# Kernel optimization log

Hardware: AMD Instinct MI355X
Metric: run time of the kernel (lower is better)

Reference implementation:

```python
import jax, jax.numpy as jnp
import numpy as np

D_MODEL = 2048
NUM_HEADS = 16
HEAD_DIM = 128
BATCH = 4
SEQ = 2048


def setup_inputs() -> dict:
    key = jax.random.key(0)
    ks = jax.random.split(key, 5)
    s = 0.02
    return {
        "x": jax.random.normal(ks[0], (BATCH, SEQ, D_MODEL), dtype=jnp.float32),
        "Wq": jax.random.normal(ks[1], (NUM_HEADS * HEAD_DIM, D_MODEL), dtype=jnp.float32) * s,
        "Wk": jax.random.normal(ks[2], (NUM_HEADS * HEAD_DIM, D_MODEL), dtype=jnp.float32) * s,
        "Wv": jax.random.normal(ks[3], (NUM_HEADS * HEAD_DIM, D_MODEL), dtype=jnp.float32) * s,
        "Wo": jax.random.normal(ks[4], (D_MODEL, NUM_HEADS * HEAD_DIM), dtype=jnp.float32) * s,
    }


def _split_heads(t):
    b, s, _ = t.shape
    return t.reshape(b, s, NUM_HEADS, HEAD_DIM).transpose(0, 2, 1, 3)  # [b,h,s,d]


def reference(x, Wq, Wk, Wv, Wo):
    # prefill: QKV proj + causal SDPA + output proj. torch Linear: x @ W.T
    q = _split_heads(x @ Wq.T)
    k = _split_heads(x @ Wk.T)
    v = _split_heads(x @ Wv.T)
    scale = 1.0 / jnp.sqrt(jnp.asarray(HEAD_DIM, dtype=x.dtype))
    scores = jnp.einsum("bhqd,bhkd->bhqk", q, k) * scale
    causal = jnp.tril(jnp.ones((SEQ, SEQ), dtype=bool))
    scores = jnp.where(causal, scores, jnp.finfo(scores.dtype).min)
    attn = jax.nn.softmax(scores, axis=-1)
    y = jnp.einsum("bhqk,bhkd->bhqd", attn, v)
    y = y.transpose(0, 2, 1, 3).reshape(x.shape[0], SEQ, NUM_HEADS * HEAD_DIM)
    y = y @ Wo.T
    return (y, k, v)
```

## Files before the change

### kernel.cpp

```cpp
#include <hip/hip_runtime.h>
#include <stdint.h>

#define DM 2048
#define NH 16
#define HD 128
#define BB 4
#define SS 2048
#define BS (BB*SS)
#define NQKV (3*DM)
#define SCQ 0.12751744565f

typedef __bf16 bf16_t;
typedef __attribute__((ext_vector_type(8))) __bf16 bf16x8;
typedef __attribute__((ext_vector_type(4))) float f32x4;
typedef __attribute__((ext_vector_type(16))) float f32x16;
typedef __attribute__((ext_vector_type(4))) float float4v;
typedef __attribute__((ext_vector_type(4))) unsigned int uint4v;
typedef __attribute__((ext_vector_type(4))) unsigned short ushort4v;
typedef __attribute__((ext_vector_type(8))) unsigned short ushort8;

__device__ __forceinline__ unsigned short f2bf(float f) {
  unsigned u = __float_as_uint(f);
  u += 0x7fffu + ((u >> 16) & 1u);
  return (unsigned short)(u >> 16);
}

__device__ __forceinline__ void gl16(const void* g, void* l) {
  __builtin_amdgcn_global_load_lds(
      (const __attribute__((address_space(1))) unsigned int*)(unsigned long long)g,
      (__attribute__((address_space(3))) unsigned int*)(unsigned int)(unsigned long long)l,
      16, 0, 0);
}

#define DSR(dst, addr, IMM)                                                   \
  asm volatile("ds_read_b128 %0, %1 offset:" IMM : "=v"(dst) : "v"(addr))

__global__ void conv_f32_bf16(const float* __restrict__ in,
                              unsigned short* __restrict__ out, int n4) {
  int i = blockIdx.x * blockDim.x + threadIdx.x;
  int stride = gridDim.x * blockDim.x;
  for (; i < n4; i += stride) {
    float4v v = ((const float4v*)in)[i];
    ushort4v o;
    o.x = f2bf(v.x); o.y = f2bf(v.y); o.z = f2bf(v.z); o.w = f2bf(v.w);
    ((ushort4v*)out)[i] = o;
  }
}

template<int MODE>
__global__ __launch_bounds__(512)
void gemmr4(const bf16_t* __restrict__ A, const bf16_t* __restrict__ Bm,
            const int K, const int N, const int nbx,
            float* __restrict__ Cf, bf16_t* __restrict__ qbf,
            bf16_t* __restrict__ kbt, float* __restrict__ kf,
            float* __restrict__ vf, bf16_t* __restrict__ vtb) {
  __shared__ bf16_t As[4][256 * 32];
  __shared__ bf16_t Bs[4][256 * 32];
  const int t = threadIdx.x, w = t >> 6, lane = t & 63;
  const int fr = lane & 15, fq = lane >> 4;
  const int cpx = gridDim.x >> 3;
  const int orig = blockIdx.x;
  const int wg = (orig & 7) * cpx + (orig >> 3);
  const int bm = wg % nbx, bn = wg / nbx;
  const int row0 = bm * 256, col0 = bn * 256;
  const int wm = (w >> 2) * 128, wn = (w & 3) * 64;

  const bf16_t* Asrc[2];
  const bf16_t* Bsrc[2];
  int dst[2];
#pragma unroll
  for (int j = 0; j < 2; ++j) {
    int u = j * 512 + t, r = u >> 2, c = u & 3;
    Asrc[j] = A + (size_t)(row0 + r) * K + ((c ^ (r & 3)) * 8);
    Bsrc[j] = Bm + (size_t)(col0 + r) * K + ((c ^ (r & 3)) * 8);
    dst[j] = u * 16;
  }
  const int NT = K >> 5;
  f32x4 acc[8][4] = {};

  const unsigned As0 = (unsigned)(unsigned long long)(const void*)&As[0][0];
  const unsigned Bs0 = (unsigned)(unsigned long long)(const void*)&Bs[0][0];
  const unsigned xorc = (unsigned)((fq ^ (fr & 3)) << 4);
  const unsigned aoff = (unsigned)((wm + fr) * 64) + xorc;
  const unsigned boff = (unsigned)((wn + fr) * 64) + xorc;

#define STAGE(TT)                                                  \
  {                                                                \
    const int sl_ = (TT) & 3;                                      \
    const size_t ko_ = (size_t)(TT) * 32;                          \
    gl16(Asrc[0] + ko_, (char*)(&As[sl_][0]) + dst[0]);            \
    gl16(Asrc[1] + ko_, (char*)(&As[sl_][0]) + dst[1]);            \
    gl16(Bsrc[0] + ko_, (char*)(&Bs[sl_][0]) + dst[0]);            \
    gl16(Bsrc[1] + ko_, (char*)(&Bs[sl_][0]) + dst[1]);            \
  }

#define MFQUAD(FI, AV)                                                        \
  acc[FI][0] = __builtin_amdgcn_mfma_f32_16x16x32_bf16(                       \
      __builtin_bit_cast(bf16x8, AV), __builtin_bit_cast(bf16x8, bv0), acc[FI][0], 0, 0, 0); \
  acc[FI][1] = __builtin_amdgcn_mfma_f32_16x16x32_bf16(                       \
      __builtin_bit_cast(bf16x8, AV), __builtin_bit_cast(bf16x8, bv1), acc[FI][1], 0, 0, 0); \
  acc[FI][2] = __builtin_amdgcn_mfma_f32_16x16x32_bf16(                       \
      __builtin_bit_cast(bf16x8, AV), __builtin_bit_cast(bf16x8, bv2), acc[FI][2], 0, 0, 0); \
  acc[FI][3] = __builtin_amdgcn_mfma_f32_16x16x32_bf16(                       \
      __builtin_bit_cast(bf16x8, AV), __builtin_bit_cast(bf16x8, bv3), acc[FI][3], 0, 0, 0);

  STAGE(0); STAGE(1); STAGE(2);

  for (int T = 0; T < NT; ++T) {
    if (T + 2 < NT) {
      asm volatile("s_waitcnt vmcnt(8)" ::: "memory");
    } else if (T + 1 < NT) {
      asm volatile("s_waitcnt vmcnt(4)" ::: "memory");
    } else {
      asm volatile("s_waitcnt vmcnt(0)" ::: "memory");
    }
    asm volatile("s_barrier" ::: "memory");
    if (T + 3 < NT) STAGE(T + 3);

    const unsigned ab = As0 + (unsigned)(T & 3) * 16384 + aoff;
    const unsigned bb = Bs0 + (unsigned)(T & 3) * 16384 + boff;
    uint4v bv0, bv1, bv2, bv3, a0, a1, a2, a3, a4, a5, a6, a7;
    DSR(bv0, bb, "0");    DSR(bv1, bb, "1024");
    DSR(bv2, bb, "2048"); DSR(bv3, bb, "3072");
    DSR(a0, ab, "0");     DSR(a1, ab, "1024");
    DSR(a2, ab, "2048");  DSR(a3, ab, "3072");
    DSR(a4, ab, "4096");  DSR(a5, ab, "5120");
    DSR(a6, ab, "6144");  DSR(a7, ab, "7168");

    asm volatile("s_waitcnt lgkmcnt(4)" ::: "memory");
    __builtin_amdgcn_sched_barrier(0);
    __builtin_amdgcn_s_setprio(1);
    MFQUAD(0, a0) MFQUAD(1, a1) MFQUAD(2, a2) MFQUAD(3, a3)
    __builtin_amdgcn_s_setprio(0);

    asm volatile("s_waitcnt lgkmcnt(0)" ::: "memory");
    __builtin_amdgcn_sched_barrier(0);
    __builtin_amdgcn_s_setprio(1);
    MFQUAD(4, a4) MFQUAD(5, a5) MFQUAD(6, a6) MFQUAD(7, a7)
    __builtin_amdgcn_s_setprio(0);
  }
#undef STAGE
#undef MFQUAD

#pragma unroll
  for (int f = 0; f < 8; ++f) {
#pragma unroll
    for (int jn = 0; jn < 4; ++jn) {
#pragma unroll
      for (int r = 0; r < 4; ++r) {
        int m = row0 + wm + f * 16 + fq * 4 + r;
        int n = col0 + wn + jn * 16 + fr;
        float v = acc[f][jn][r];
        if (MODE == 0) {
          Cf[(size_t)m * N + n] = v;
        } else {
          int b = m >> 11, s = m & 2047;
          if (n < DM) {
            int h = n >> 7, d = n & 127;
            qbf[(((size_t)(b * NH + h)) * SS + s) * HD + d] = (bf16_t)(v * SCQ);
          } else if (n < 2 * DM) {
            int nn = n - DM, h = nn >> 7, d = nn & 127;
            size_t o = (((size_t)(b * NH + h)) * SS + s) * HD + d;
            kbt[o] = (bf16_t)v;
            kf[o] = v;
          } else {
            int nn = n - 2 * DM, h = nn >> 7, d = nn & 127;
            size_t o = (((size_t)(b * NH + h)) * SS + s) * HD + d;
            vf[o] = v;
            vtb[((size_t)(b * NH + h)) * (HD * SS) + (size_t)d * SS + s] = (bf16_t)v;
          }
        }
      }
    }
  }
}

__global__ __launch_bounds__(256, 2)
void attn_fwd4(const bf16_t* __restrict__ qbf, const bf16_t* __restrict__ kbf,
               const bf16_t* __restrict__ vt, bf16_t* __restrict__ aout) {
  __shared__ bf16_t Ks[2][64 * 128];
  __shared__ bf16_t Vs[2][64 * 128];
  const int t = threadIdx.x, w = t >> 6, lane = t & 63;
  const int l31 = lane & 31, hi = lane >> 5;
  const int orig = blockIdx.x;
  const int wg = (orig & 7) * 128 + (orig >> 3);
  const int bh = wg >> 4;
  const int qt = 15 - (wg & 15);
  const int q0 = qt * 128;
  const int nt = 2 * qt + 2;
  const size_t bh_off = (size_t)bh * SS * HD;
  const char* kbase = (const char*)(kbf + bh_off);
  const char* vbase = (const char*)(vt + bh_off);

  const char* ksrc[4];
  const char* vsrc[4];
#pragma unroll
  for (int i = 0; i < 4; ++i) {
    int r = (w * 4 + i) * 4 + (lane >> 4);
    int c = (lane & 15) ^ (r & 15);
    ksrc[i] = kbase + r * 256 + c * 16;
    int d = 2 * r + (c >> 3);
    vsrc[i] = vbase + (size_t)d * (SS * 2) + (c & 7) * 16;
  }

  bf16x8 qfr[8];
  {
    const char* qrow = (const char*)(qbf + bh_off + (size_t)(q0 + w * 32 + l31) * HD);
#pragma unroll
    for (int ds = 0; ds < 8; ++ds)
      qfr[ds] = *(const bf16x8*)(qrow + ds * 32 + hi * 16);
  }

#pragma unroll
  for (int i = 0; i < 4; ++i) {
    gl16(ksrc[i], (char*)(&Ks[0][0]) + (w * 4 + i) * 1024);
    gl16(vsrc[i], (char*)(&Vs[0][0]) + (w * 4 + i) * 1024);
    ksrc[i] += 16384;
    vsrc[i] += 128;
  }

  float mrow = -3.0e38f, lrow = 0.f;
  f32x16 accO[4] = {};

  auto make_pa = [&](const f32x16& sv, bf16x8& paA, bf16x8& paB) {
    unsigned W[8];
#pragma unroll
    for (int m = 0; m < 8; ++m) {
      float lo = sv[2 * m], hh = sv[2 * m + 1];
      asm("v_cvt_pk_bf16_f32 %0, %1, %2" : "=v"(W[m]) : "v"(lo), "v"(hh));
    }
#pragma unroll
    for (int g = 0; g < 2; ++g) {
      unsigned A = W[4 * g], B = W[4 * g + 1], C = W[4 * g + 2], D = W[4 * g + 3];
      unsigned xA = (unsigned)__shfl_xor((int)A, 32, 64);
      unsigned xB = (unsigned)__shfl_xor((int)B, 32, 64);
      unsigned xC = (unsigned)__shfl_xor((int)C, 32, 64);
      unsigned xD = (unsigned)__shfl_xor((int)D, 32, 64);
      uint4v u;
      u.x = hi ? xC : A;
      u.y = hi ? xD : B;
      u.z = hi ? C : xA;
      u.w = hi ? D : xB;
      if (g == 0) paA = __builtin_bit_cast(bf16x8, u);
      else        paB = __builtin_bit_cast(bf16x8, u);
    }
  };

  for (int kt = 0; kt < nt; ++kt) {
    const int cur = kt & 1;
    __syncthreads();

    if (kt + 1 < nt) {
#pragma unroll
      for (int i = 0; i < 4; ++i) {
        gl16(ksrc[i], (char*)(&Ks[cur ^ 1][0]) + (w * 4 + i) * 1024);
        gl16(vsrc[i], (char*)(&Vs[cur ^ 1][0]) + (w * 4 + i) * 1024);
        ksrc[i] += 16384;
        vsrc[i] += 128;
      }
    }

    const char* kl = (const char*)&Ks[cur][0];
    f32x16 s0 = {}, s1 = {};
    const int rck = l31 & 15;
    __builtin_amdgcn_s_setprio(1);
#pragma unroll
    for (int ds = 0; ds < 8; ++ds) {
      int ch = ((2 * ds + hi) ^ rck) << 4;
      bf16x8 kf0 = *(const bf16x8*)(kl + l31 * 256 + ch);
      s0 = __builtin_amdgcn_mfma_f32_32x32x16_bf16(kf0, qfr[ds], s0, 0, 0, 0);
      bf16x8 kf1 = *(const bf16x8*)(kl + (32 + l31) * 256 + ch);
      s1 = __builtin_amdgcn_mfma_f32_32x32x16_bf16(kf1, qfr[ds], s1, 0, 0, 0);
    }
    __builtin_amdgcn_s_setprio(0);

    const int kv0 = kt * 64;
    if (kt >= 2 * qt) {
      const int qg = q0 + w * 32 + l31;
#pragma unroll
      for (int r = 0; r < 16; ++r) {
        int klo = kv0 + (r & 3) + 8 * (r >> 2) + 4 * hi;
        if (klo > qg) s0[r] = -3.0e38f;
        if (klo + 32 > qg) s1[r] = -3.0e38f;
      }
    }
    float rm = s0[0];
#pragma unroll
    for (int r = 1; r < 16; ++r) rm = fmaxf(rm, s0[r]);
#pragma unroll
    for (int r = 0; r < 16; ++r) rm = fmaxf(rm, s1[r]);
    rm = fmaxf(rm, __shfl_xor(rm, 32, 64));
    if (__ballot(rm > mrow + 8.0f)) {
      float mnew = fmaxf(mrow, rm);
      float fct = __builtin_amdgcn_exp2f(mrow - mnew);
      mrow = mnew;
      lrow *= fct;
#pragma unroll
      for (int r = 0; r < 16; ++r) {
        float f = __shfl(fct, (r & 3) + 8 * (r >> 2) + 4 * hi, 64);
        accO[0][r] *= f; accO[1][r] *= f; accO[2][r] *= f; accO[3][r] *= f;
      }
    }
    float ss = 0.f;
#pragma unroll
    for (int r = 0; r < 16; ++r) { float p = __builtin_amdgcn_exp2f(s0[r] - mrow); s0[r] = p; ss += p; }
#pragma unroll
    for (int r = 0; r < 16; ++r) { float p = __builtin_amdgcn_exp2f(s1[r] - mrow); s1[r] = p; ss += p; }
    ss += __shfl_xor(ss, 32, 64);
    lrow += ss;

    bf16x8 pa00, pa01, pa10, pa11;
    make_pa(s0, pa00, pa01);
    make_pa(s1, pa10, pa11);

    const char* vl = (const char*)&Vs[cur][0];
    __builtin_amdgcn_s_setprio(1);
#pragma unroll
    for (int dt = 0; dt < 4; ++dt) {
      int R = dt * 16 + (l31 >> 1);
      int cb = (l31 & 1) << 3;
      int rx = R & 15;
      bf16x8 v00 = *(const bf16x8*)(vl + R * 256 + (((cb + 0 + hi) ^ rx) << 4));
      accO[dt] = __builtin_amdgcn_mfma_f32_32x32x16_bf16(pa00, v00, accO[dt], 0, 0, 0);
      bf16x8 v01 = *(const bf16x8*)(vl + R * 256 + (((cb + 2 + hi) ^ rx) << 4));
      accO[dt] = __builtin_amdgcn_mfma_f32_32x32x16_bf16(pa01, v01, accO[dt], 0, 0, 0);
      bf16x8 v10 = *(const bf16x8*)(vl + R * 256 + (((cb + 4 + hi) ^ rx) << 4));
      accO[dt] = __builtin_amdgcn_mfma_f32_32x32x16_bf16(pa10, v10, accO[dt], 0, 0, 0);
      bf16x8 v11 = *(const bf16x8*)(vl + R * 256 + (((cb + 6 + hi) ^ rx) << 4));
      accO[dt] = __builtin_amdgcn_mfma_f32_32x32x16_bf16(pa11, v11, accO[dt], 0, 0, 0);
    }
    __builtin_amdgcn_s_setprio(0);
  }

  const int b = bh >> 4, h = bh & 15;
#pragma unroll
  for (int r = 0; r < 16; ++r) {
    int qr = (r & 3) + 8 * (r >> 2) + 4 * hi;
    float inv = __builtin_amdgcn_rcpf(__shfl(lrow, qr, 64));
    int srow = q0 + w * 32 + qr;
    bf16_t* orow = aout + ((size_t)(b * SS + srow)) * DM + h * HD + l31;
    orow[0]  = (bf16_t)(accO[0][r] * inv);
    orow[32] = (bf16_t)(accO[1][r] * inv);
    orow[64] = (bf16_t)(accO[2][r] * inv);
    orow[96] = (bf16_t)(accO[3][r] * inv);
  }
}

extern "C" void kernel_launch(void* const* d_in, const int* in_sizes, int n_in,
                              void* d_out, int out_size, void* d_ws, size_t ws_size,
                              hipStream_t stream) {
  (void)in_sizes; (void)n_in; (void)out_size; (void)ws_size;
  const float* x  = (const float*)d_in[0];
  const float* Wq = (const float*)d_in[1];
  const float* Wk = (const float*)d_in[2];
  const float* Wv = (const float*)d_in[3];
  const float* Wo = (const float*)d_in[4];

  float* y  = (float*)d_out;
  float* kf = y + (size_t)BS * DM;
  float* vf = kf + (size_t)BS * DM;

  char* ws = (char*)d_ws;
  bf16_t* xbf  = (bf16_t*)ws;
  bf16_t* abf  = xbf;
  bf16_t* qbf  = (bf16_t*)(ws + (size_t)32 * 1024 * 1024);
  bf16_t* wobf = qbf;
  bf16_t* wqkv = (bf16_t*)(ws + (size_t)64 * 1024 * 1024);
  bf16_t* kbt  = (bf16_t*)y;
  bf16_t* vtb  = (bf16_t*)((char*)y + (size_t)32 * 1024 * 1024);

  conv_f32_bf16<<<2048, 256, 0, stream>>>(x, (unsigned short*)xbf, BS * DM / 4);
  conv_f32_bf16<<<512, 256, 0, stream>>>(Wq, (unsigned short*)wqkv, DM * DM / 4);
  conv_f32_bf16<<<512, 256, 0, stream>>>(Wk, (unsigned short*)(wqkv + (size_t)DM * DM), DM * DM / 4);
  conv_f32_bf16<<<512, 256, 0, stream>>>(Wv, (unsigned short*)(wqkv + 2 * (size_t)DM * DM), DM * DM / 4);

  gemmr4<1><<<768, 512, 0, stream>>>(
      xbf, wqkv, DM, NQKV, 32, nullptr, qbf, kbt, kf, vf, vtb);

  attn_fwd4<<<1024, 256, 0, stream>>>(qbf, kbt, vtb, abf);

  conv_f32_bf16<<<512, 256, 0, stream>>>(Wo, (unsigned short*)wobf, DM * DM / 4);

  gemmr4<0><<<256, 512, 0, stream>>>(
      abf, wobf, DM, DM, 32, y, nullptr, nullptr, nullptr, nullptr, nullptr);
}
```

Before: 520.0 us.

## Fuse conversions, add 128-tile QKV GEMM, use permlane32 swap in attention

Merges the five fp32-to-bf16 conversion launches into one kernel, with the Wo copy given its own workspace slot. The QKV projection moves to a new simpler 128x128-tile GEMM with a single LDS buffer, whose epilogue branches on the block's column range rather than per element. The attention P-fragment repack swaps shuffles and selects for v_permlane32_swap instructions. The LDS swizzle in the remaining GEMM changes to an (r>>1) pattern. The new QKV GEMM drops the 4-stage pipelining of the old kernel, so it may expose global-load latency.

```diff
diff --git a/kernel.cpp b/kernel.cpp
--- a/kernel.cpp
+++ b/kernel.cpp
@@ -35,15 +35,110 @@
 #define DSR(dst, addr, IMM)                                                   \
   asm volatile("ds_read_b128 %0, %1 offset:" IMM : "=v"(dst) : "v"(addr))
 
-__global__ void conv_f32_bf16(const float* __restrict__ in,
-                              unsigned short* __restrict__ out, int n4) {
+__global__ void conv_all(const float* __restrict__ x,  const float* __restrict__ wq,
+                         const float* __restrict__ wk, const float* __restrict__ wv,
+                         const float* __restrict__ wo,
+                         unsigned short* __restrict__ xbf,
+                         unsigned short* __restrict__ wqkv,
+                         unsigned short* __restrict__ wobf) {
+  const int NX = BS * DM / 4;
+  const int NW = DM * DM / 4;
   int i = blockIdx.x * blockDim.x + threadIdx.x;
   int stride = gridDim.x * blockDim.x;
-  for (; i < n4; i += stride) {
-    float4v v = ((const float4v*)in)[i];
+  for (; i < NX + 4 * NW; i += stride) {
+    const float4v* src;
+    ushort4v* dst;
+    if (i < NX)               { src = (const float4v*)x  + i;            dst = (ushort4v*)xbf + i; }
+    else if (i < NX + NW)     { int j = i - NX;          src = (const float4v*)wq + j; dst = (ushort4v*)wqkv + j; }
+    else if (i < NX + 2 * NW) { int j = i - NX - NW;     src = (const float4v*)wk + j; dst = (ushort4v*)wqkv + NW + j; }
+    else if (i < NX + 3 * NW) { int j = i - NX - 2 * NW; src = (const float4v*)wv + j; dst = (ushort4v*)wqkv + 2 * NW + j; }
+    else                      { int j = i - NX - 3 * NW; src = (const float4v*)wo + j; dst = (ushort4v*)wobf + j; }
+    float4v v = *src;
     ushort4v o;
     o.x = f2bf(v.x); o.y = f2bf(v.y); o.z = f2bf(v.z); o.w = f2bf(v.w);
-    ((ushort4v*)out)[i] = o;
+    *dst = o;
+  }
+}
+
+__global__ __launch_bounds__(256)
+void gemm128q(const bf16_t* __restrict__ A, const bf16_t* __restrict__ Bm,
+              bf16_t* __restrict__ qbf, bf16_t* __restrict__ kbt,
+              float* __restrict__ kf, float* __restrict__ vf,
+              bf16_t* __restrict__ vtb) {
+  __shared__ bf16_t As[128 * 32];
+  __shared__ bf16_t Bs[128 * 32];
+  const int t = threadIdx.x, w = t >> 6, lane = t & 63;
+  const int fr = lane & 15, fq = lane >> 4;
+  const int cpx = gridDim.x >> 3;
+  const int orig = blockIdx.x;
+  const int wg = (orig & 7) * cpx + (orig >> 3);
+  const int bm = wg & 63, bn = wg >> 6;
+  const int row0 = bm * 128, col0 = bn * 128;
+  const int wm = (w >> 1) * 64, wn = (w & 1) * 64;
+  const int K = DM;
+
+  const bf16_t *A0, *A1, *B0, *B1;
+  {
+    int u0 = t, r0 = u0 >> 2, c0 = u0 & 3;
+    int u1 = 256 + t, r1 = u1 >> 2, c1 = u1 & 3;
+    A0 = A + (size_t)(row0 + r0) * K + ((c0 ^ ((r0 >> 1) & 3)) * 8);
+    A1 = A + (size_t)(row0 + r1) * K + ((c1 ^ ((r1 >> 1) & 3)) * 8);
+    B0 = Bm + (size_t)(col0 + r0) * K + ((c0 ^ ((r0 >> 1) & 3)) * 8);
+    B1 = Bm + (size_t)(col0 + r1) * K + ((c1 ^ ((r1 >> 1) & 3)) * 8);
+  }
+  const int d0 = t * 16, d1 = (256 + t) * 16;
+  const int swz = ((fq ^ ((fr >> 1) & 3)) * 8);
+
+  f32x4 acc[4][4] = {};
+
+  for (int kk = 0; kk < K; kk += 32) {
+    __syncthreads();
+    gl16(A0 + kk, (char*)As + d0);
+    gl16(A1 + kk, (char*)As + d1);
+    gl16(B0 + kk, (char*)Bs + d0);
+    gl16(B1 + kk, (char*)Bs + d1);
+    __syncthreads();
+    bf16x8 af[4], bfv[4];
+#pragma unroll
+    for (int f = 0; f < 4; ++f) {
+      af[f]  = *(const bf16x8*)(As + (wm + f * 16 + fr) * 32 + swz);
+      bfv[f] = *(const bf16x8*)(Bs + (wn + f * 16 + fr) * 32 + swz);
+    }
+    __builtin_amdgcn_s_setprio(1);
+#pragma unroll
+    for (int i = 0; i < 4; ++i)
+#pragma unroll
+      for (int jn = 0; jn < 4; ++jn)
+        acc[i][jn] = __builtin_amdgcn_mfma_f32_16x16x32_bf16(af[i], bfv[jn], acc[i][jn], 0, 0, 0);
+    __builtin_amdgcn_s_setprio(0);
+  }
+
+#pragma unroll
+  for (int i = 0; i < 4; ++i) {
+#pragma unroll
+    for (int jn = 0; jn < 4; ++jn) {
+#pragma unroll
+      for (int r = 0; r < 4; ++r) {
+        int m = row0 + wm + i * 16 + fq * 4 + r;
+        int n = col0 + wn + jn * 16 + fr;
+        float v = acc[i][jn][r];
+        int b = m >> 11, s = m & 2047;
+        if (col0 < DM) {
+          int h = n >> 7, d = n & 127;
+          qbf[(((size_t)(b * NH + h)) * SS + s) * HD + d] = (bf16_t)(v * SCQ);
+        } else if (col0 < 2 * DM) {
+          int nn = n - DM, h = nn >> 7, d = nn & 127;
+          size_t o = (((size_t)(b * NH + h)) * SS + s) * HD + d;
+          kbt[o] = (bf16_t)v;
+          kf[o] = v;
+        } else {
+          int nn = n - 2 * DM, h = nn >> 7, d = nn & 127;
+          size_t o = (((size_t)(b * NH + h)) * SS + s) * HD + d;
+          vf[o] = v;
+          vtb[((size_t)(b * NH + h)) * (HD * SS) + (size_t)d * SS + s] = (bf16_t)v;
+        }
+      }
+    }
   }
 }
 
@@ -51,9 +146,7 @@
 __global__ __launch_bounds__(512)
 void gemmr4(const bf16_t* __restrict__ A, const bf16_t* __restrict__ Bm,
             const int K, const int N, const int nbx,
-            float* __restrict__ Cf, bf16_t* __restrict__ qbf,
-            bf16_t* __restrict__ kbt, float* __restrict__ kf,
-            float* __restrict__ vf, bf16_t* __restrict__ vtb) {
+            float* __restrict__ Cf) {
   __shared__ bf16_t As[4][256 * 32];
   __shared__ bf16_t Bs[4][256 * 32];
   const int t = threadIdx.x, w = t >> 6, lane = t & 63;
@@ -71,8 +164,8 @@
 #pragma unroll
   for (int j = 0; j < 2; ++j) {
     int u = j * 512 + t, r = u >> 2, c = u & 3;
-    Asrc[j] = A + (size_t)(row0 + r) * K + ((c ^ (r & 3)) * 8);
-    Bsrc[j] = Bm + (size_t)(col0 + r) * K + ((c ^ (r & 3)) * 8);
+    Asrc[j] = A + (size_t)(row0 + r) * K + ((c ^ ((r >> 1) & 3)) * 8);
+    Bsrc[j] = Bm + (size_t)(col0 + r) * K + ((c ^ ((r >> 1) & 3)) * 8);
     dst[j] = u * 16;
   }
   const int NT = K >> 5;
@@ -80,7 +173,7 @@
 
   const unsigned As0 = (unsigned)(unsigned long long)(const void*)&As[0][0];
   const unsigned Bs0 = (unsigned)(unsigned long long)(const void*)&Bs[0][0];
-  const unsigned xorc = (unsigned)((fq ^ (fr & 3)) << 4);
+  const unsigned xorc = (unsigned)((fq ^ ((fr >> 1) & 3)) << 4);
   const unsigned aoff = (unsigned)((wm + fr) * 64) + xorc;
   const unsigned boff = (unsigned)((wn + fr) * 64) + xorc;
 
@@ -150,33 +243,14 @@
       for (int r = 0; r < 4; ++r) {
         int m = row0 + wm + f * 16 + fq * 4 + r;
         int n = col0 + wn + jn * 16 + fr;
-        float v = acc[f][jn][r];
-        if (MODE == 0) {
-          Cf[(size_t)m * N + n] = v;
-        } else {
-          int b = m >> 11, s = m & 2047;
-          if (n < DM) {
-            int h = n >> 7, d = n & 127;
-            qbf[(((size_t)(b * NH + h)) * SS + s) * HD + d] = (bf16_t)(v * SCQ);
-          } else if (n < 2 * DM) {
-            int nn = n - DM, h = nn >> 7, d = nn & 127;
-            size_t o = (((size_t)(b * NH + h)) * SS + s) * HD + d;
-            kbt[o] = (bf16_t)v;
-            kf[o] = v;
-          } else {
-            int nn = n - 2 * DM, h = nn >> 7, d = nn & 127;
-            size_t o = (((size_t)(b * NH + h)) * SS + s) * HD + d;
-            vf[o] = v;
-            vtb[((size_t)(b * NH + h)) * (HD * SS) + (size_t)d * SS + s] = (bf16_t)v;
-          }
-        }
+        Cf[(size_t)m * N + n] = acc[f][jn][r];
       }
     }
   }
 }
 
 __global__ __launch_bounds__(256, 2)
-void attn_fwd4(const bf16_t* __restrict__ qbf, const bf16_t* __restrict__ kbf,
+void attn_fwd5(const bf16_t* __restrict__ qbf, const bf16_t* __restrict__ kbf,
                const bf16_t* __restrict__ vt, bf16_t* __restrict__ aout) {
   __shared__ bf16_t Ks[2][64 * 128];
   __shared__ bf16_t Vs[2][64 * 128];
@@ -229,21 +303,14 @@
       float lo = sv[2 * m], hh = sv[2 * m + 1];
       asm("v_cvt_pk_bf16_f32 %0, %1, %2" : "=v"(W[m]) : "v"(lo), "v"(hh));
     }
-#pragma unroll
-    for (int g = 0; g < 2; ++g) {
-      unsigned A = W[4 * g], B = W[4 * g + 1], C = W[4 * g + 2], D = W[4 * g + 3];
-      unsigned xA = (unsigned)__shfl_xor((int)A, 32, 64);
-      unsigned xB = (unsigned)__shfl_xor((int)B, 32, 64);
-      unsigned xC = (unsigned)__shfl_xor((int)C, 32, 64);
-      unsigned xD = (unsigned)__shfl_xor((int)D, 32, 64);
-      uint4v u;
-      u.x = hi ? xC : A;
-      u.y = hi ? xD : B;
-      u.z = hi ? C : xA;
-      u.w = hi ? D : xB;
-      if (g == 0) paA = __builtin_bit_cast(bf16x8, u);
-      else        paB = __builtin_bit_cast(bf16x8, u);
-    }
+    asm volatile("v_permlane32_swap_b32 %0, %1" : "+v"(W[0]), "+v"(W[2]));
+    asm volatile("v_permlane32_swap_b32 %0, %1" : "+v"(W[1]), "+v"(W[3]));
+    asm volatile("v_permlane32_swap_b32 %0, %1" : "+v"(W[4]), "+v"(W[6]));
+    asm volatile("v_permlane32_swap_b32 %0, %1" : "+v"(W[5]), "+v"(W[7]));
+    uint4v u0; u0.x = W[0]; u0.y = W[1]; u0.z = W[2]; u0.w = W[3];
+    paA = __builtin_bit_cast(bf16x8, u0);
+    uint4v u1; u1.x = W[4]; u1.y = W[5]; u1.z = W[6]; u1.w = W[7];
+    paB = __builtin_bit_cast(bf16x8, u1);
   };
 
   for (int kt = 0; kt < nt; ++kt) {
@@ -364,23 +431,18 @@
   bf16_t* xbf  = (bf16_t*)ws;
   bf16_t* abf  = xbf;
   bf16_t* qbf  = (bf16_t*)(ws + (size_t)32 * 1024 * 1024);
-  bf16_t* wobf = qbf;
   bf16_t* wqkv = (bf16_t*)(ws + (size_t)64 * 1024 * 1024);
+  bf16_t* wobf = (bf16_t*)(ws + (size_t)88 * 1024 * 1024);
   bf16_t* kbt  = (bf16_t*)y;
   bf16_t* vtb  = (bf16_t*)((char*)y + (size_t)32 * 1024 * 1024);
 
-  conv_f32_bf16<<<2048, 256, 0, stream>>>(x, (unsigned short*)xbf, BS * DM / 4);
-  conv_f32_bf16<<<512, 256, 0, stream>>>(Wq, (unsigned short*)wqkv, DM * DM / 4);
-  conv_f32_bf16<<<512, 256, 0, stream>>>(Wk, (unsigned short*)(wqkv + (size_t)DM * DM), DM * DM / 4);
-  conv_f32_bf16<<<512, 256, 0, stream>>>(Wv, (unsigned short*)(wqkv + 2 * (size_t)DM * DM), DM * DM / 4);
-
-  gemmr4<1><<<768, 512, 0, stream>>>(
-      xbf, wqkv, DM, NQKV, 32, nullptr, qbf, kbt, kf, vf, vtb);
-
-  attn_fwd4<<<1024, 256, 0, stream>>>(qbf, kbt, vtb, abf);
-
-  conv_f32_bf16<<<512, 256, 0, stream>>>(Wo, (unsigned short*)wobf, DM * DM / 4);
-
-  gemmr4<0><<<256, 512, 0, stream>>>(
-      abf, wobf, DM, DM, 32, y, nullptr, nullptr, nullptr, nullptr, nullptr);
-}
+  conv_all<<<2048, 256, 0, stream>>>(x, Wq, Wk, Wv, Wo,
+                                     (unsigned short*)xbf, (unsigned short*)wqkv,
+                                     (unsigned short*)wobf);
+
+  gemm128q<<<3072, 256, 0, stream>>>(xbf, wqkv, qbf, kbt, kf, vf, vtb);
+
+  attn_fwd5<<<1024, 256, 0, stream>>>(qbf, kbt, vtb, abf);
+
+  gemmr4<0><<<256, 512, 0, stream>>>(abf, wobf, DM, DM, 32, y);
+}
```

New measurement: 607.6 us. +16.9%, slower.
